# Kernel optimization log

Hardware: AMD Instinct MI355X
Metric: run time of the kernel (lower is better)

The kernel has to match this reference:

```python
import jax, jax.numpy as jnp
import numpy as np

K = 20          # args.k
NEG = 0.2       # LeakyReLU negative slope

def lrelu(x):
    return jnp.where(x >= 0, x, NEG * x)

def bn(x, s, b):
    # eval-mode batchnorm folded into per-channel affine; channel axis = 1
    sh = (1, -1) + (1,) * (x.ndim - 2)
    return x * s.reshape(sh) + b.reshape(sh)

def se(x, w1, w2):
    # Squeeze-and-Excite on (B, C, N, k)
    y = jnp.mean(x, axis=(2, 3))                      # (B, C)
    y = jax.nn.sigmoid(jax.nn.relu(y @ w1.T) @ w2.T)  # (B, C)
    return x * y[:, :, None, None]

def graph_feature(x):
    # x: (B, C, N) -> edge features (B, 2C, N, K)
    xx = jnp.sum(x * x, axis=1)                        # (B, N)
    inner = jnp.einsum('bcn,bcm->bnm', x, x)           # (B, N, N)
    dist = -xx[:, :, None] + 2.0 * inner - xx[:, None, :]
    idx = jax.lax.top_k(dist, K)[1]                    # (B, N, K) nearest (incl. self)
    xt = jnp.transpose(x, (0, 2, 1))                   # (B, N, C)
    nbr = jax.vmap(lambda t, i: t[i])(xt, idx)         # (B, N, K, C)
    ctr = xt[:, :, None, :]
    out = jnp.concatenate([nbr - ctr, jnp.broadcast_to(ctr, nbr.shape)], axis=3)
    return jnp.transpose(out, (0, 3, 1, 2))

def edge_block(x, w, s, b, w1, w2):
    # get_graph_feature -> 1x1 conv -> BN -> SE -> LeakyReLU -> max over k
    g = graph_feature(x)                               # (B, 2C, N, K)
    h = jnp.einsum('bcnk,oc->bonk', g, w)
    h = lrelu(se(bn(h, s, b), w1, w2))
    return jnp.max(h, axis=-1)                         # (B, O, N)

def forward(x, conv1_w, conv2_w, conv3_w, conv4_w, conv5_w,
            bn1_s, bn1_b, bn2_s, bn2_b, bn3_s, bn3_b, bn4_s, bn4_b, bn5_s, bn5_b,
            se1_w1, se1_w2, se2_w1, se2_w2, se3_w1, se3_w2, se4_w1, se4_w2,
            res1_w, res2_w, res3_w,
            lin1_w, bn6_s, bn6_b, lin2_w, lin2_b, bn7_s, bn7_b, lin3_w, lin3_b):
    x1 = edge_block(x, conv1_w, bn1_s, bn1_b, se1_w1, se1_w2)                 # (B,512,N)
    x2 = edge_block(x1, conv2_w, bn2_s, bn2_b, se2_w1, se2_w2)
    x2 = x2 + jnp.einsum('bcn,oc->bon', x1, res1_w)                           # (B,512,N)
    x3 = edge_block(x2, conv3_w, bn3_s, bn3_b, se3_w1, se3_w2)
    x3 = x3 + jnp.einsum('bcn,oc->bon', x2, res2_w)                           # (B,1024,N)
    x4 = edge_block(x3, conv4_w, bn4_s, bn4_b, se4_w1, se4_w2)
    x4 = x4 + jnp.einsum('bcn,oc->bon', x3, res3_w)                           # (B,1024,N)
    h = jnp.concatenate([x1, x2, x3, x4], axis=1)                             # (B,3072,N)
    h = lrelu(bn(jnp.einsum('bcn,oc->bon', h, conv5_w), bn5_s, bn5_b))        # (B,2048,N)
    f = jnp.concatenate([jnp.max(h, axis=-1), jnp.mean(h, axis=-1)], axis=1)  # (B,4096)
    f = lrelu(bn(f @ lin1_w.T, bn6_s, bn6_b))       # dropout is eval-mode identity
    f = lrelu(bn(f @ lin2_w.T + lin2_b, bn7_s, bn7_b))
    return f @ lin3_w.T + lin3_b                    # (B,40)

def setup_inputs():
    ks = jax.random.split(jax.random.key(0), 40)
    B, N = 16, 128
    f32 = jnp.float32
    def w(i, shape, s=0.02):
        return jax.random.normal(ks[i], shape, f32) * s
    def bns(i, c):
        return 1.0 + 0.1 * jax.random.normal(ks[i], (c,), f32)
    def bnb(i, c):
        return 0.1 * jax.random.normal(ks[i], (c,), f32)
    return {
        'x': jax.random.normal(ks[0], (B, 512, N), f32),
        'conv1_w': w(1, (512, 1024)),
        'conv2_w': w(2, (512, 1024)),
        'conv3_w': w(3, (1024, 1024)),
        'conv4_w': w(4, (1024, 2048)),
        'conv5_w': w(5, (2048, 3072)),
        'bn1_s': bns(6, 512), 'bn1_b': bnb(7, 512),
        'bn2_s': bns(8, 512), 'bn2_b': bnb(9, 512),
        'bn3_s': bns(10, 1024), 'bn3_b': bnb(11, 1024),
        'bn4_s': bns(12, 1024), 'bn4_b': bnb(13, 1024),
        'bn5_s': bns(14, 2048), 'bn5_b': bnb(15, 2048),
        'se1_w1': w(16, (32, 512), 0.05), 'se1_w2': w(17, (512, 32), 0.05),
        'se2_w1': w(18, (32, 512), 0.05), 'se2_w2': w(19, (512, 32), 0.05),
        'se3_w1': w(20, (64, 1024), 0.05), 'se3_w2': w(21, (1024, 64), 0.05),
        'se4_w1': w(22, (64, 1024), 0.05), 'se4_w2': w(23, (1024, 64), 0.05),
        'res1_w': w(24, (512, 512)),
        'res2_w': w(25, (1024, 512)),
        'res3_w': w(26, (1024, 1024)),
        'lin1_w': w(27, (512, 4096)),
        'bn6_s': bns(28, 512), 'bn6_b': bnb(29, 512),
        'lin2_w': w(30, (256, 512)), 'lin2_b': bnb(31, 256),
        'bn7_s': bns(32, 256), 'bn7_b': bnb(33, 256),
        'lin3_w': w(34, (40, 256)), 'lin3_b': bnb(35, 40),
    }

def reference(x, conv1_w, conv2_w, conv3_w, conv4_w, conv5_w,
              bn1_s, bn1_b, bn2_s, bn2_b, bn3_s, bn3_b, bn4_s, bn4_b, bn5_s, bn5_b,
              se1_w1, se1_w2, se2_w1, se2_w2, se3_w1, se3_w2, se4_w1, se4_w2,
              res1_w, res2_w, res3_w,
              lin1_w, bn6_s, bn6_b, lin2_w, lin2_b, bn7_s, bn7_b, lin3_w, lin3_b):
    return forward(x, conv1_w, conv2_w, conv3_w, conv4_w, conv5_w,
                   bn1_s, bn1_b, bn2_s, bn2_b, bn3_s, bn3_b, bn4_s, bn4_b, bn5_s, bn5_b,
                   se1_w1, se1_w2, se2_w1, se2_w2, se3_w1, se3_w2, se4_w1, se4_w2,
                   res1_w, res2_w, res3_w,
                   lin1_w, bn6_s, bn6_b, lin2_w, lin2_b, bn7_s, bn7_b, lin3_w, lin3_b)
```

## Files before the change

kernel.cpp:

```cpp
#include <hip/hip_runtime.h>
#include <hip/hip_bf16.h>


#define BN_ALL 2048
typedef __hip_bfloat16 bf16;
typedef __attribute__((ext_vector_type(8))) short short8;
typedef __attribute__((ext_vector_type(4))) float float4v;

__device__ __forceinline__ float b2f(bf16 v) { return __bfloat162float(v); }
__device__ __forceinline__ float lrelu(float v) { return v >= 0.f ? v : 0.2f * v; }
__device__ __forceinline__ short f2bs(float v) {
    bf16 h = __float2bfloat16(v);
    return *reinterpret_cast<short*>(&h);
}

__device__ __forceinline__ float ldin(const void* p, size_t i, int isb) {
    return isb ? __bfloat162float(((const bf16*)p)[i]) : ((const float*)p)[i];
}

__device__ __forceinline__ float ld1(const float* p) { return *p; }
__device__ __forceinline__ float ld1(const bf16* p)  { return __bfloat162float(*p); }
__device__ __forceinline__ void st1(float* p, float v) { *p = v; }
__device__ __forceinline__ void st1(bf16* p, float v)  { *p = __float2bfloat16(v); }
__device__ __forceinline__ short ldbs(const float* p) { return f2bs(*p); }
__device__ __forceinline__ short ldbs(const bf16* p)  { return *(const short*)p; }

__global__ __launch_bounds__(256) void detect_dtype(const void* __restrict__ x, int* __restrict__ flag) {
    const unsigned* u = (const unsigned*)x;
    int sane = 0;
    for (int i = threadIdx.x; i < 4096; i += 256) {
        unsigned e = (u[i] >> 23) & 0xFF;
        sane += (e >= 87 && e <= 167) ? 1 : 0;
    }
    __shared__ int sh[256];
    sh[threadIdx.x] = sane;
    __syncthreads();
    for (int off = 128; off > 0; off >>= 1) {
        if (threadIdx.x < off) sh[threadIdx.x] += sh[threadIdx.x + off];
        __syncthreads();
    }
    if (threadIdx.x == 0) *flag = (sh[0] < 2048) ? 1 : 0;
}

__global__ __launch_bounds__(256) void convert_kp(const void* __restrict__ x, bf16* __restrict__ X0,
                                                  const int* __restrict__ dflag) {
    int isb = *dflag;
    int item = blockIdx.x * 256 + threadIdx.x;
    int cg = item >> 11, bn = item & 2047;
    int b = bn >> 7, n = bn & 127;
    short8 pk;
#pragma unroll
    for (int j = 0; j < 8; ++j)
        pk[j] = f2bs(ldin(x, ((size_t)(b * 512 + cg * 8 + j)) * 128 + n, isb));
    *(short8*)((short*)X0 + ((size_t)cg * BN_ALL + bn) * 8) = pk;
}

__global__ __launch_bounds__(256) void gram_k(const bf16* __restrict__ X, int C,
                                              float* __restrict__ G) {
    __shared__ short Bsm[2][4096];
    int tid = threadIdx.x;
    int b = blockIdx.x;
    int lane = tid & 63, wv = tid >> 6, wm = wv & 1, wn = wv >> 1;
    int lq = lane >> 4, lr = lane & 15;
    int KC = C >> 5;
    const short* Xs = (const short*)X;

    float4v acc[4][4];
#pragma unroll
    for (int i = 0; i < 4; i++)
#pragma unroll
        for (int j = 0; j < 4; j++) acc[i][j] = (float4v){0.f, 0.f, 0.f, 0.f};

    short8 br2[2];
#pragma unroll
    for (int it = 0; it < 2; ++it) {
        int i = tid + it * 256;
        int q = i >> 7, c = i & 127;
        *(short8*)&Bsm[0][(size_t)i * 8] =
            *(const short8*)(Xs + ((size_t)q * BN_ALL + b * 128 + c) * 8);
    }
    __syncthreads();

    int p = 0;
    for (int kc = 0; kc < KC; ++kc) {
        if (kc + 1 < KC) {
#pragma unroll
            for (int it = 0; it < 2; ++it) {
                int i = tid + it * 256;
                int q = i >> 7, c = i & 127;
                br2[it] = *(const short8*)(Xs + ((size_t)((kc + 1) * 4 + q) * BN_ALL + b * 128 + c) * 8);
            }
        }
        short8 av[4], bv[4];
#pragma unroll
        for (int mt = 0; mt < 4; ++mt)
            av[mt] = *(const short8*)&Bsm[p][(size_t)((lq << 7) + wm * 64 + mt * 16 + lr) * 8];
#pragma unroll
        for (int nt = 0; nt < 4; ++nt)
            bv[nt] = *(const short8*)&Bsm[p][(size_t)((lq << 7) + wn * 64 + nt * 16 + lr) * 8];
#pragma unroll
        for (int mt = 0; mt < 4; ++mt)
#pragma unroll
            for (int nt = 0; nt < 4; ++nt)
                acc[mt][nt] = __builtin_amdgcn_mfma_f32_16x16x32_bf16(av[mt], bv[nt], acc[mt][nt], 0, 0, 0);
        if (kc + 1 < KC) {
#pragma unroll
            for (int it = 0; it < 2; ++it)
                *(short8*)&Bsm[p ^ 1][(size_t)(tid + it * 256) * 8] = br2[it];
        }
        __syncthreads();
        p ^= 1;
    }

    float* Gb = G + (size_t)b * 16384;
#pragma unroll
    for (int mt = 0; mt < 4; ++mt)
#pragma unroll
        for (int r = 0; r < 4; ++r) {
            int row = wm * 64 + mt * 16 + lq * 4 + r;
#pragma unroll
            for (int nt = 0; nt < 4; ++nt) {
                int col = wn * 64 + nt * 16 + lr;
                Gb[row * 128 + col] = acc[mt][nt][r];
            }
        }
}

__global__ __launch_bounds__(256) void topk_k(const float* __restrict__ G, int* __restrict__ idx) {
    int gw = (blockIdx.x * 256 + threadIdx.x) >> 6;
    int lane = threadIdx.x & 63;
    int b = gw >> 7, n = gw & 127;
    const float* Gb = G + (size_t)b * 16384;
    float g0 = Gb[n * 128 + lane];
    float g1 = Gb[n * 128 + 64 + lane];
    float dnn = Gb[n * 129];
    float dm0 = Gb[lane * 129];
    float dm1 = Gb[(64 + lane) * 129];
    float d0 = 2.f * g0 - dnn - dm0;
    float d1 = 2.f * g1 - dnn - dm1;
#pragma unroll
    for (int k = 0; k < 20; ++k) {
        float v; int i;
        if (d1 > d0) { v = d1; i = 64 + lane; } else { v = d0; i = lane; }
#pragma unroll
        for (int off = 1; off < 64; off <<= 1) {
            float ov = __shfl_xor(v, off, 64);
            int   oi = __shfl_xor(i, off, 64);
            if (ov > v || (ov == v && oi < i)) { v = ov; i = oi; }
        }
        if (lane == 0) idx[gw * 20 + k] = i;
        if (i < 64) { if (lane == i) d0 = -3.0e38f; }
        else        { if (lane == i - 64) d1 = -3.0e38f; }
    }
}

template <typename S>
__global__ __launch_bounds__(128) void knn_topk(const S* __restrict__ X, int C, int* __restrict__ idx) {
// ... 32 lines not shown
        }
        if (m == 0) { idx[blockIdx.x * 20 + k] = ri[0]; dist[ri[0]] = -3.0e38f; }
    }
}

__global__ __launch_bounds__(256) void pack_w(const void* __restrict__ w, int ldw,
                                              const void* __restrict__ res, int Cin, int O,
                                              int Mtot, int K, short* __restrict__ out,
                                              const int* __restrict__ dflag) {
    int isb = *dflag;
    int item = blockIdx.x * 256 + threadIdx.x;
    if (item >= Mtot * (K >> 3)) return;
    int m_local = item & 127;
    int rest = item >> 7;
    int q = rest & 3; rest >>= 2;
    int KC = K >> 5;
    int kc = rest % KC, tm = rest / KC;
    int grow = tm * 128 + m_local;
    int k = kc * 32 + q * 8;
    const void* src; size_t base; int dif = 0;
    if (grow < O)          { src = w;   base = (size_t)grow * ldw + k; }
    else if (grow < 2 * O) { src = w;   base = (size_t)(grow - O) * ldw + k; dif = 1; }
    else                   { src = res; base = (size_t)(grow - 2 * O) * Cin + k; }
    short8 pk;
#pragma unroll
    for (int j = 0; j < 8; ++j) {
        float v = ldin(src, base + j, isb);
        if (dif) v = ldin(src, base + Cin + j, isb) - v;
        pk[j] = f2bs(v);
    }
    *(short8*)&out[(size_t)item * 8] = pk;
}

__global__ __launch_bounds__(256) void gemm_pk(const short* __restrict__ packA,
                                               const bf16* __restrict__ X, float* __restrict__ Cm, int K,
                                               const void* __restrict__ bnS, const void* __restrict__ bnB,
                                               int act, const int* __restrict__ dflag) {
    __shared__ short Asm[2][4096];
    __shared__ short Bsm[2][2048];
    int tid = threadIdx.x;
    int bm  = blockIdx.x << 7;
    int bn0 = blockIdx.y << 6;
    int lane = tid & 63, wv = tid >> 6, wm = wv & 1, wn = wv >> 1;
    int lq = lane >> 4, lr = lane & 15;
    int KC = K >> 5;
    const short* abase = packA + (size_t)blockIdx.x * KC * 4096;
    const short* Xs = (const short*)X;
    int bq = tid >> 6, bc = tid & 63;

    float4v acc[4][2];
#pragma unroll
    for (int i = 0; i < 4; i++)
#pragma unroll
        for (int j = 0; j < 2; j++) acc[i][j] = (float4v){0.f, 0.f, 0.f, 0.f};

    short8 ar[2], brv;

#pragma unroll
    for (int it = 0; it < 2; ++it)
        ar[it] = *(const short8*)&abase[(size_t)(tid + it * 256) * 8];
    brv = *(const short8*)(Xs + ((size_t)bq * BN_ALL + bn0 + bc) * 8);
#pragma unroll
    for (int it = 0; it < 2; ++it)
        *(short8*)&Asm[0][(size_t)(tid + it * 256) * 8] = ar[it];
    *(short8*)&Bsm[0][(size_t)tid * 8] = brv;
    __syncthreads();

    int p = 0;
    for (int kc = 0; kc < KC; ++kc) {
        if (kc + 1 < KC) {
            const short* ab = abase + (size_t)(kc + 1) * 4096;
#pragma unroll
            for (int it = 0; it < 2; ++it)
                ar[it] = *(const short8*)&ab[(size_t)(tid + it * 256) * 8];
            brv = *(const short8*)(Xs + ((size_t)((kc + 1) * 4 + bq) * BN_ALL + bn0 + bc) * 8);
        }
        short8 av[4], bv[2];
#pragma unroll
        for (int mt = 0; mt < 4; ++mt)
            av[mt] = *(const short8*)&Asm[p][(size_t)((lq << 7) + wm * 64 + mt * 16 + lr) * 8];
#pragma unroll
        for (int nt = 0; nt < 2; ++nt)
            bv[nt] = *(const short8*)&Bsm[p][(size_t)((lq << 6) + wn * 32 + nt * 16 + lr) * 8];
#pragma unroll
        for (int mt = 0; mt < 4; ++mt)
#pragma unroll
            for (int nt = 0; nt < 2; ++nt)
                acc[mt][nt] = __builtin_amdgcn_mfma_f32_16x16x32_bf16(av[mt], bv[nt], acc[mt][nt], 0, 0, 0);
        if (kc + 1 < KC) {
#pragma unroll
            for (int it = 0; it < 2; ++it)
                *(short8*)&Asm[p ^ 1][(size_t)(tid + it * 256) * 8] = ar[it];
            *(short8*)&Bsm[p ^ 1][(size_t)tid * 8] = brv;
        }
        __syncthreads();
        p ^= 1;
    }

    int isb = *dflag;
#pragma unroll
    for (int mt = 0; mt < 4; ++mt) {
#pragma unroll
        for (int r = 0; r < 4; ++r) {
            int row = bm + wm * 64 + mt * 16 + lq * 4 + r;
            float s = 1.f, bb = 0.f;
            if (bnS) { s = ldin(bnS, row, isb); bb = ldin(bnB, row, isb); }
#pragma unroll
            for (int nt = 0; nt < 2; ++nt) {
                int col = bn0 + wn * 32 + nt * 16 + lr;
                float v = acc[mt][nt][r];
                if (bnS) v = v * s + bb;
                if (act) v = lrelu(v);
                Cm[(size_t)row * BN_ALL + col] = v;
            }
        }
    }
}

template <typename S>
__global__ __launch_bounds__(256) void gemm_mfma(const void* __restrict__ w, int ldw,
                                                 const void* __restrict__ res, int Cin, int O,
                                                 const S* __restrict__ X, S* __restrict__ Cm, int K,
                                                 const void* __restrict__ bnS, const void* __restrict__ bnB,
                                                 int act, const int* __restrict__ dflag) {
    int isb = *dflag;
    __shared__ short Asm[4096];
    __shared__ short Bsm[4096];
    int tid = threadIdx.x;
    int bm  = blockIdx.x << 7;
    int bn0 = blockIdx.y << 7;
    int lane = tid & 63, wv = tid >> 6;
    int wm = wv & 1, wn = wv >> 1;
    int lq = lane >> 4, lr = lane & 15;

    float4v acc[4][4];
#pragma unroll
    for (int i = 0; i < 4; i++)
#pragma unroll
        for (int j = 0; j < 4; j++) acc[i][j] = (float4v){0.f, 0.f, 0.f, 0.f};

    for (int k0 = 0; k0 < K; k0 += 32) {
#pragma unroll
        for (int it = 0; it < 2; ++it) {
            int i = tid + it * 256;
            int m = i >> 2, q = i & 3;
            int grow = bm + m;
            const void* asrc; size_t abase; int dif = 0;
            if (grow < O)          { asrc = w;   abase = (size_t)grow * ldw; }
            else if (grow < 2 * O) { asrc = w;   abase = (size_t)(grow - O) * ldw; dif = 1; }
            else                   { asrc = res; abase = (size_t)(grow - 2 * O) * Cin; }
            size_t kk = (size_t)k0 + q * 8;
// ... 135 lines not shown
    int item = blockIdx.x * 256 + threadIdx.x;
    int og = item >> 11, bn = item & 2047;
    int b = bn >> 7;
    short8 pk;
#pragma unroll
    for (int j = 0; j < 8; ++j) {
        int r = og * 8 + j;
        float v = Y[b * O + r] * PS[(size_t)r * BN_ALL + bn];
        if (useR) v += PS[(size_t)(2 * O + r) * BN_ALL + bn];
        pk[j] = f2bs(v);
    }
    *(short8*)((short*)Xdst + ((size_t)og * BN_ALL + bn) * 8) = pk;
}

template <typename SP, typename SD>
__global__ __launch_bounds__(256) void finalize(const SP* __restrict__ PS, const float* __restrict__ Y,
                                                int useR, SD* __restrict__ Xdst, int O) {
    int tid = blockIdx.x * 256 + threadIdx.x;
    int o = tid >> 11, bn = tid & 2047;
    int b = bn >> 7;
    float v = Y[b * O + o] * ld1(PS + tid);
    if (useR) v += ld1(PS + (size_t)(2 * O + o) * BN_ALL + bn);
    st1(Xdst + tid, v);
}

template <typename S>
__global__ __launch_bounds__(256) void convert_x(const void* __restrict__ x, S* __restrict__ X0,
                                                 const int* __restrict__ dflag) {
    int isb = *dflag;
    int tid = blockIdx.x * 256 + threadIdx.x;
    int c = tid >> 11, bn = tid & 2047;
    int b = bn >> 7, n = bn & 127;
    st1(X0 + tid, ldin(x, (size_t)(b * 512 + c) * 128 + n, isb));
}

template <typename S>
__global__ __launch_bounds__(128) void pool5(const S* __restrict__ H, float* __restrict__ f) {
    int m = blockIdx.x, b = blockIdx.y, n = threadIdx.x;
    float v = ld1(H + (size_t)m * BN_ALL + b * 128 + n);
    __shared__ float rmx[128], rsm[128];
    rmx[n] = v; rsm[n] = v;
    __syncthreads();
    for (int off = 64; off > 0; off >>= 1) {
        if (n < off) { rmx[n] = fmaxf(rmx[n], rmx[n + off]); rsm[n] += rsm[n + off]; }
        __syncthreads();
    }
    if (n == 0) {
        f[b * 4096 + m] = rmx[0];
        f[b * 4096 + 2048 + m] = rsm[0] * (1.f / 128.f);
    }
}

__global__ __launch_bounds__(256) void head_k(const float* __restrict__ in, const void* __restrict__ W,
                                              const void* __restrict__ bias, const void* __restrict__ bns,
                                              const void* __restrict__ bnb, float* __restrict__ outf,
                                              void* __restrict__ outb, int Kd, int Od, int act,
                                              const int* __restrict__ dflag) {
    int isb = *dflag;
    int gw = (blockIdx.x * 256 + threadIdx.x) >> 6;
    int lane = threadIdx.x & 63;
    if (gw >= 16 * Od) return;
    int b = gw / Od, o = gw - b * Od;
    const float* iv = in + b * Kd;
    float acc = 0.f;
    for (int k = lane; k < Kd; k += 64) acc += iv[k] * ldin(W, (size_t)o * Kd + k, isb);
    for (int off = 32; off > 0; off >>= 1) acc += __shfl_xor(acc, off, 64);
// ... 29 lines not shown
    const void* se3w1 = d_in[20], * se3w2 = d_in[21];                       \
    const void* se4w1 = d_in[22], * se4w2 = d_in[23];                       \
    const void* res1w = d_in[24]; const void* res2w = d_in[25];             \
    const void* res3w = d_in[26]; const void* lin1w = d_in[27];             \
    const void* bn6s = d_in[28], * bn6b = d_in[29];                         \
    const void* lin2w = d_in[30], * lin2b = d_in[31];                       \
    const void* bn7s = d_in[32], * bn7b = d_in[33];                         \
    const void* lin3w = d_in[34], * lin3b = d_in[35];

static void run_net_packed(void* const* d_in, void* d_out, void* d_ws, hipStream_t stream) {
    UNPACK_INPUTS();
    float* WS = (float*)d_ws;
    float* PS   = WS;
    bf16*  XC   = (bf16*)(WS + 6291456);
    short* PACK = (short*)(WS + 12582912);
    float* MB = WS + 15728640;
    float* YB = MB + 16384;
    float* FB = YB + 16384;
    float* F1 = FB + 65536;
    float* F2 = F1 + 8192;
    int* IDX  = (int*)(F2 + 4096);
    int* DFLAG = IDX + 40960;
    float* ZB = (float*)(DFLAG + 16);
    bf16*  X0 = (bf16*)(PS + (size_t)2048 * BN_ALL);
    float* GRAM = PS;
    bf16* X1 = XC;
    bf16* X2 = XC + (size_t)512 * BN_ALL;
    bf16* X3 = XC + (size_t)1024 * BN_ALL;
    bf16* X4 = XC + (size_t)2048 * BN_ALL;

    detect_dtype<<<1, 256, 0, stream>>>(x_in, DFLAG);
    convert_kp<<<512, 256, 0, stream>>>(x_in, X0, DFLAG);

    gram_k<<<16, 256, 0, stream>>>(X0, 512, GRAM);
    topk_k<<<512, 256, 0, stream>>>(GRAM, IDX);
    pack_w<<<256, 256, 0, stream>>>(conv1w, 1024, nullptr, 512, 512, 1024, 512, PACK, DFLAG);
    gemm_pk<<<dim3(8, 32), 256, 0, stream>>>(PACK, X0, PS, 512, nullptr, nullptr, 0, DFLAG);
    gather_pool<float><<<dim3(512, 16), 128, 0, stream>>>(PS, IDX, bn1s, bn1b, MB, 512, DFLAG);
    se1_k<<<128, 256, 0, stream>>>(MB, se1w1, ZB, 512, 32, DFLAG);
    se2_k<<<2048, 256, 0, stream>>>(ZB, se1w2, YB, 512, 32, DFLAG);
    finalize_kp<<<512, 256, 0, stream>>>(PS, YB, 0, X1, 512);

    gram_k<<<16, 256, 0, stream>>>(X1, 512, GRAM);
    topk_k<<<512, 256, 0, stream>>>(GRAM, IDX);
    pack_w<<<384, 256, 0, stream>>>(conv2w, 1024, res1w, 512, 512, 1536, 512, PACK, DFLAG);
    gemm_pk<<<dim3(12, 32), 256, 0, stream>>>(PACK, X1, PS, 512, nullptr, nullptr, 0, DFLAG);
    gather_pool<float><<<dim3(512, 16), 128, 0, stream>>>(PS, IDX, bn2s, bn2b, MB, 512, DFLAG);
    se1_k<<<128, 256, 0, stream>>>(MB, se2w1, ZB, 512, 32, DFLAG);
    se2_k<<<2048, 256, 0, stream>>>(ZB, se2w2, YB, 512, 32, DFLAG);
    finalize_kp<<<512, 256, 0, stream>>>(PS, YB, 1, X2, 512);

    gram_k<<<16, 256, 0, stream>>>(X2, 512, GRAM);
    topk_k<<<512, 256, 0, stream>>>(GRAM, IDX);
    pack_w<<<768, 256, 0, stream>>>(conv3w, 1024, res2w, 512, 1024, 3072, 512, PACK, DFLAG);
    gemm_pk<<<dim3(24, 32), 256, 0, stream>>>(PACK, X2, PS, 512, nullptr, nullptr, 0, DFLAG);
    gather_pool<float><<<dim3(1024, 16), 128, 0, stream>>>(PS, IDX, bn3s, bn3b, MB, 1024, DFLAG);
    se1_k<<<256, 256, 0, stream>>>(MB, se3w1, ZB, 1024, 64, DFLAG);
    se2_k<<<4096, 256, 0, stream>>>(ZB, se3w2, YB, 1024, 64, DFLAG);
    finalize_kp<<<1024, 256, 0, stream>>>(PS, YB, 1, X3, 1024);

    gram_k<<<16, 256, 0, stream>>>(X3, 1024, GRAM);
    topk_k<<<512, 256, 0, stream>>>(GRAM, IDX);
    pack_w<<<1536, 256, 0, stream>>>(conv4w, 2048, res3w, 1024, 1024, 3072, 1024, PACK, DFLAG);
    gemm_pk<<<dim3(24, 32), 256, 0, stream>>>(PACK, X3, PS, 1024, nullptr, nullptr, 0, DFLAG);
    gather_pool<float><<<dim3(1024, 16), 128, 0, stream>>>(PS, IDX, bn4s, bn4b, MB, 1024, DFLAG);
    se1_k<<<256, 256, 0, stream>>>(MB, se4w1, ZB, 1024, 64, DFLAG);
    se2_k<<<4096, 256, 0, stream>>>(ZB, se4w2, YB, 1024, 64, DFLAG);
    finalize_kp<<<1024, 256, 0, stream>>>(PS, YB, 1, X4, 1024);

    pack_w<<<3072, 256, 0, stream>>>(conv5w, 3072, nullptr, 3072, 2048, 2048, 3072, PACK, DFLAG);
    gemm_pk<<<dim3(16, 32), 256, 0, stream>>>(PACK, XC, PS, 3072, bn5s, bn5b, 1, DFLAG);
    pool5<float><<<dim3(2048, 16), 128, 0, stream>>>(PS, FB);

    head_k<<<2048, 256, 0, stream>>>(FB, lin1w, nullptr, bn6s, bn6b, F1, nullptr, 4096, 512, 1, DFLAG);
    head_k<<<1024, 256, 0, stream>>>(F1, lin2w, lin2b, bn7s, bn7b, F2, nullptr, 512, 256, 1, DFLAG);
    head_k<<<160, 256, 0, stream>>>(F2, lin3w, lin3b, nullptr, nullptr, nullptr, d_out, 256, 40, 0, DFLAG);
}

template <typename S>
static void run_net(void* const* d_in, void* d_out, void* d_ws, hipStream_t stream) {
    UNPACK_INPUTS();
    const size_t RC = (size_t)3072 * BN_ALL;
    S* PS = (S*)d_ws;
    S* XC = PS + RC;
    S* X0 = PS + (size_t)2048 * BN_ALL;
    float* MB = (float*)(XC + RC);
    float* YB = MB + 16 * 1024;
    float* FB = YB + 16 * 1024;
    float* F1 = FB + 16 * 4096;
    float* F2 = F1 + 16 * 512;
    int* IDX  = (int*)(F2 + 16 * 256);
    int* DFLAG = IDX + 16 * 128 * 20;

    S* X1 = XC;
    S* X2 = XC + (size_t)512 * BN_ALL;
    S* X3 = XC + (size_t)1024 * BN_ALL;
    S* X4 = XC + (size_t)2048 * BN_ALL;

    detect_dtype<<<1, 256, 0, stream>>>(x_in, DFLAG);
    convert_x<S><<<4096, 256, 0, stream>>>(x_in, X0, DFLAG);

    knn_topk<S><<<2048, 128, 0, stream>>>(X0, 512, IDX);
    gemm_mfma<S><<<dim3(8, 16), 256, 0, stream>>>(conv1w, 1024, nullptr, 512, 512, X0, PS, 512, nullptr, nullptr, 0, DFLAG);
    gather_pool<S><<<dim3(512, 16), 128, 0, stream>>>(PS, IDX, bn1s, bn1b, MB, 512, DFLAG);
    se_k<<<16, 256, 0, stream>>>(MB, se1w1, se1w2, YB, 512, 32, DFLAG);
// ... 47 lines not shown
```

Before: 626.1 us.

## Split gram kernel into column strips and split-K the conv5 GEMM

```diff
diff --git a/kernel.cpp b/kernel.cpp
--- a/kernel.cpp
+++ b/kernel.cpp
@@ -42,6 +42,12 @@
     if (threadIdx.x == 0) *flag = (sh[0] < 2048) ? 1 : 0;
 }
 
+__global__ __launch_bounds__(256) void zero_ps(float* __restrict__ P) {
+    int i = blockIdx.x * 256 + threadIdx.x;
+    float4 z = {0.f, 0.f, 0.f, 0.f};
+    *(float4*)(P + (size_t)i * 4) = z;
+}
+
 __global__ __launch_bounds__(256) void convert_kp(const void* __restrict__ x, bf16* __restrict__ X0,
                                                   const int* __restrict__ dflag) {
     int isb = *dflag;
@@ -59,17 +65,15 @@
                                               float* __restrict__ G) {
     __shared__ short Bsm[2][4096];
     int tid = threadIdx.x;
-    int b = blockIdx.x;
+    int b = blockIdx.x, strip = blockIdx.y;
     int lane = tid & 63, wv = tid >> 6, wm = wv & 1, wn = wv >> 1;
     int lq = lane >> 4, lr = lane & 15;
     int KC = C >> 5;
     const short* Xs = (const short*)X;
 
-    float4v acc[4][4];
-#pragma unroll
-    for (int i = 0; i < 4; i++)
-#pragma unroll
-        for (int j = 0; j < 4; j++) acc[i][j] = (float4v){0.f, 0.f, 0.f, 0.f};
+    float4v acc[4];
+#pragma unroll
+    for (int i = 0; i < 4; i++) acc[i] = (float4v){0.f, 0.f, 0.f, 0.f};
 
     short8 br2[2];
 #pragma unroll
@@ -91,18 +95,14 @@
                 br2[it] = *(const short8*)(Xs + ((size_t)((kc + 1) * 4 + q) * BN_ALL + b * 128 + c) * 8);
             }
         }
-        short8 av[4], bv[4];
+        short8 av[4], bv;
 #pragma unroll
         for (int mt = 0; mt < 4; ++mt)
             av[mt] = *(const short8*)&Bsm[p][(size_t)((lq << 7) + wm * 64 + mt * 16 + lr) * 8];
-#pragma unroll
-        for (int nt = 0; nt < 4; ++nt)
-            bv[nt] = *(const short8*)&Bsm[p][(size_t)((lq << 7) + wn * 64 + nt * 16 + lr) * 8];
+        bv = *(const short8*)&Bsm[p][(size_t)((lq << 7) + strip * 32 + wn * 16 + lr) * 8];
 #pragma unroll
         for (int mt = 0; mt < 4; ++mt)
-#pragma unroll
-            for (int nt = 0; nt < 4; ++nt)
-                acc[mt][nt] = __builtin_amdgcn_mfma_f32_16x16x32_bf16(av[mt], bv[nt], acc[mt][nt], 0, 0, 0);
+            acc[mt] = __builtin_amdgcn_mfma_f32_16x16x32_bf16(av[mt], bv, acc[mt], 0, 0, 0);
         if (kc + 1 < KC) {
 #pragma unroll
             for (int it = 0; it < 2; ++it)
@@ -118,11 +118,8 @@
 #pragma unroll
         for (int r = 0; r < 4; ++r) {
             int row = wm * 64 + mt * 16 + lq * 4 + r;
-#pragma unroll
-            for (int nt = 0; nt < 4; ++nt) {
-                int col = wn * 64 + nt * 16 + lr;
-                Gb[row * 128 + col] = acc[mt][nt][r];
-            }
+            int col = strip * 32 + wn * 16 + lr;
+            Gb[row * 128 + col] = acc[mt][r];
         }
 }
 
@@ -306,6 +303,86 @@
     }
 }
 
+__global__ __launch_bounds__(256) void gemm_sk(const short* __restrict__ packA,
+                                               const bf16* __restrict__ X, float* __restrict__ Cm,
+                                               int K, int KH) {
+    __shared__ short Asm[2][4096];
+    __shared__ short Bsm[2][2048];
+    int tid = threadIdx.x;
+    int bm  = blockIdx.x << 7;
+    int bn0 = blockIdx.y << 6;
+    int kh  = blockIdx.z;
+    int lane = tid & 63, wv = tid >> 6, wm = wv & 1, wn = wv >> 1;
+    int lq = lane >> 4, lr = lane & 15;
+    int KCfull = K >> 5;
+    int KC = KCfull / KH;
+    int kc0 = kh * KC;
+    const short* abase = packA + ((size_t)blockIdx.x * KCfull + kc0) * 4096;
+    const short* Xs = (const short*)X;
+    int bq = tid >> 6, bc = tid & 63;
+
+    float4v acc[4][2];
+#pragma unroll
+    for (int i = 0; i < 4; i++)
+#pragma unroll
+        for (int j = 0; j < 2; j++) acc[i][j] = (float4v){0.f, 0.f, 0.f, 0.f};
+
+    short8 ar[2], brv;
+
+#pragma unroll
+    for (int it = 0; it < 2; ++it)
+        ar[it] = *(const short8*)&abase[(size_t)(tid + it * 256) * 8];
+    brv = *(const short8*)(Xs + ((size_t)(kc0 * 4 + bq) * BN_ALL + bn0 + bc) * 8);
+#pragma unroll
+    for (int it = 0; it < 2; ++it)
+        *(short8*)&Asm[0][(size_t)(tid + it * 256) * 8] = ar[it];
+    *(short8*)&Bsm[0][(size_t)tid * 8] = brv;
+    __syncthreads();
+
+    int p = 0;
+    for (int kc = 0; kc < KC; ++kc) {
+        if (kc + 1 < KC) {
+            const short* ab = abase + (size_t)(kc + 1) * 4096;
+#pragma unroll
+            for (int it = 0; it < 2; ++it)
+                ar[it] = *(const short8*)&ab[(size_t)(tid + it * 256) * 8];
+            brv = *(const short8*)(Xs + ((size_t)((kc0 + kc + 1) * 4 + bq) * BN_ALL + bn0 + bc) * 8);
+        }
+        short8 av[4], bv[2];
+#pragma unroll
+        for (int mt = 0; mt < 4; ++mt)
+            av[mt] = *(const short8*)&Asm[p][(size_t)((lq << 7) + wm * 64 + mt * 16 + lr) * 8];
+#pragma unroll
+        for (int nt = 0; nt < 2; ++nt)
+            bv[nt] = *(const short8*)&Bsm[p][(size_t)((lq << 6) + wn * 32 + nt * 16 + lr) * 8];
+#pragma unroll
+        for (int mt = 0; mt < 4; ++mt)
+#pragma unroll
+            for (int nt = 0; nt < 2; ++nt)
+                acc[mt][nt] = __builtin_amdgcn_mfma_f32_16x16x32_bf16(av[mt], bv[nt], acc[mt][nt], 0, 0, 0);
+        if (kc + 1 < KC) {
+#pragma unroll
+            for (int it = 0; it < 2; ++it)
+                *(short8*)&Asm[p ^ 1][(size_t)(tid + it * 256) * 8] = ar[it];
+            *(short8*)&Bsm[p ^ 1][(size_t)tid * 8] = brv;
+        }
+        __syncthreads();
+        p ^= 1;
+    }
+
+#pragma unroll
+    for (int mt = 0; mt < 4; ++mt)
+#pragma unroll
+        for (int r = 0; r < 4; ++r) {
+            int row = bm + wm * 64 + mt * 16 + lq * 4 + r;
+#pragma unroll
+            for (int nt = 0; nt < 2; ++nt) {
+                int col = bn0 + wn * 32 + nt * 16 + lr;
+                atomicAdd(Cm + (size_t)row * BN_ALL + col, acc[mt][nt][r]);
+            }
+        }
+}
+
 template <typename S>
 __global__ __launch_bounds__(256) void gemm_mfma(const void* __restrict__ w, int ldw,
                                                  const void* __restrict__ res, int Cin, int O,
@@ -507,6 +584,26 @@
     int c = tid >> 11, bn = tid & 2047;
     int b = bn >> 7, n = bn & 127;
     st1(X0 + tid, ldin(x, (size_t)(b * 512 + c) * 128 + n, isb));
+}
+
+__global__ __launch_bounds__(128) void pool5_bn(const float* __restrict__ H, float* __restrict__ f,
+                                                const void* __restrict__ bns, const void* __restrict__ bnb,
+                                                const int* __restrict__ dflag) {
+    int isb = *dflag;
+    int m = blockIdx.x, b = blockIdx.y, n = threadIdx.x;
+    float s = ldin(bns, m, isb), bb = ldin(bnb, m, isb);
+    float v = lrelu(H[(size_t)m * BN_ALL + b * 128 + n] * s + bb);
+    __shared__ float rmx[128], rsm[128];
+    rmx[n] = v; rsm[n] = v;
+    __syncthreads();
+    for (int off = 64; off > 0; off >>= 1) {
+        if (n < off) { rmx[n] = fmaxf(rmx[n], rmx[n + off]); rsm[n] += rsm[n + off]; }
+        __syncthreads();
+    }
+    if (n == 0) {
+        f[b * 4096 + m] = rmx[0];
+        f[b * 4096 + 2048 + m] = rsm[0] * (1.f / 128.f);
+    }
 }
 
 template <typename S>
@@ -602,7 +699,7 @@
     detect_dtype<<<1, 256, 0, stream>>>(x_in, DFLAG);
     convert_kp<<<512, 256, 0, stream>>>(x_in, X0, DFLAG);
 
-    gram_k<<<16, 256, 0, stream>>>(X0, 512, GRAM);
+    gram_k<<<dim3(16, 4), 256, 0, stream>>>(X0, 512, GRAM);
     topk_k<<<512, 256, 0, stream>>>(GRAM, IDX);
     pack_w<<<256, 256, 0, stream>>>(conv1w, 1024, nullptr, 512, 512, 1024, 512, PACK, DFLAG);
     gemm_pk<<<dim3(8, 32), 256, 0, stream>>>(PACK, X0, PS, 512, nullptr, nullptr, 0, DFLAG);
@@ -611,7 +708,7 @@
     se2_k<<<2048, 256, 0, stream>>>(ZB, se1w2, YB, 512, 32, DFLAG);
     finalize_kp<<<512, 256, 0, stream>>>(PS, YB, 0, X1, 512);
 
-    gram_k<<<16, 256, 0, stream>>>(X1, 512, GRAM);
+    gram_k<<<dim3(16, 4), 256, 0, stream>>>(X1, 512, GRAM);
     topk_k<<<512, 256, 0, stream>>>(GRAM, IDX);
     pack_w<<<384, 256, 0, stream>>>(conv2w, 1024, res1w, 512, 512, 1536, 512, PACK, DFLAG);
     gemm_pk<<<dim3(12, 32), 256, 0, stream>>>(PACK, X1, PS, 512, nullptr, nullptr, 0, DFLAG);
@@ -620,7 +717,7 @@
     se2_k<<<2048, 256, 0, stream>>>(ZB, se2w2, YB, 512, 32, DFLAG);
     finalize_kp<<<512, 256, 0, stream>>>(PS, YB, 1, X2, 512);
 
-    gram_k<<<16, 256, 0, stream>>>(X2, 512, GRAM);
+    gram_k<<<dim3(16, 4), 256, 0, stream>>>(X2, 512, GRAM);
     topk_k<<<512, 256, 0, stream>>>(GRAM, IDX);
     pack_w<<<768, 256, 0, stream>>>(conv3w, 1024, res2w, 512, 1024, 3072, 512, PACK, DFLAG);
     gemm_pk<<<dim3(24, 32), 256, 0, stream>>>(PACK, X2, PS, 512, nullptr, nullptr, 0, DFLAG);
@@ -629,7 +726,7 @@
     se2_k<<<4096, 256, 0, stream>>>(ZB, se3w2, YB, 1024, 64, DFLAG);
     finalize_kp<<<1024, 256, 0, stream>>>(PS, YB, 1, X3, 1024);
 
-    gram_k<<<16, 256, 0, stream>>>(X3, 1024, GRAM);
+    gram_k<<<dim3(16, 4), 256, 0, stream>>>(X3, 1024, GRAM);
     topk_k<<<512, 256, 0, stream>>>(GRAM, IDX);
     pack_w<<<1536, 256, 0, stream>>>(conv4w, 2048, res3w, 1024, 1024, 3072, 1024, PACK, DFLAG);
     gemm_pk<<<dim3(24, 32), 256, 0, stream>>>(PACK, X3, PS, 1024, nullptr, nullptr, 0, DFLAG);
@@ -639,8 +736,9 @@
     finalize_kp<<<1024, 256, 0, stream>>>(PS, YB, 1, X4, 1024);
 
     pack_w<<<3072, 256, 0, stream>>>(conv5w, 3072, nullptr, 3072, 2048, 2048, 3072, PACK, DFLAG);
-    gemm_pk<<<dim3(16, 32), 256, 0, stream>>>(PACK, XC, PS, 3072, bn5s, bn5b, 1, DFLAG);
-    pool5<float><<<dim3(2048, 16), 128, 0, stream>>>(PS, FB);
+    zero_ps<<<4096, 256, 0, stream>>>(PS);
+    gemm_sk<<<dim3(16, 32, 2), 256, 0, stream>>>(PACK, XC, PS, 3072, 2);
+    pool5_bn<<<dim3(2048, 16), 128, 0, stream>>>(PS, FB, bn5s, bn5b, DFLAG);
 
     head_k<<<2048, 256, 0, stream>>>(FB, lin1w, nullptr, bn6s, bn6b, F1, nullptr, 4096, 512, 1, DFLAG);
     head_k<<<1024, 256, 0, stream>>>(F1, lin2w, lin2b, bn7s, bn7b, F2, nullptr, 512, 256, 1, DFLAG);
```

New measurement: 637.7 us. Within noise of the previous version (+1.9%).

## Split gram kernel into column strips and enlarge GEMM N-tile to 128

Applied to the files above, without the earlier changes.

```diff
diff --git a/kernel.cpp b/kernel.cpp
--- a/kernel.cpp
+++ b/kernel.cpp
@@ -59,17 +59,15 @@
                                               float* __restrict__ G) {
     __shared__ short Bsm[2][4096];
     int tid = threadIdx.x;
-    int b = blockIdx.x;
+    int b = blockIdx.x, strip = blockIdx.y;
     int lane = tid & 63, wv = tid >> 6, wm = wv & 1, wn = wv >> 1;
     int lq = lane >> 4, lr = lane & 15;
     int KC = C >> 5;
     const short* Xs = (const short*)X;
 
-    float4v acc[4][4];
-#pragma unroll
-    for (int i = 0; i < 4; i++)
-#pragma unroll
-        for (int j = 0; j < 4; j++) acc[i][j] = (float4v){0.f, 0.f, 0.f, 0.f};
+    float4v acc[4];
+#pragma unroll
+    for (int i = 0; i < 4; i++) acc[i] = (float4v){0.f, 0.f, 0.f, 0.f};
 
     short8 br2[2];
 #pragma unroll
@@ -91,18 +89,14 @@
                 br2[it] = *(const short8*)(Xs + ((size_t)((kc + 1) * 4 + q) * BN_ALL + b * 128 + c) * 8);
             }
         }
-        short8 av[4], bv[4];
+        short8 av[4], bv;
 #pragma unroll
         for (int mt = 0; mt < 4; ++mt)
             av[mt] = *(const short8*)&Bsm[p][(size_t)((lq << 7) + wm * 64 + mt * 16 + lr) * 8];
-#pragma unroll
-        for (int nt = 0; nt < 4; ++nt)
-            bv[nt] = *(const short8*)&Bsm[p][(size_t)((lq << 7) + wn * 64 + nt * 16 + lr) * 8];
+        bv = *(const short8*)&Bsm[p][(size_t)((lq << 7) + strip * 32 + wn * 16 + lr) * 8];
 #pragma unroll
         for (int mt = 0; mt < 4; ++mt)
-#pragma unroll
-            for (int nt = 0; nt < 4; ++nt)
-                acc[mt][nt] = __builtin_amdgcn_mfma_f32_16x16x32_bf16(av[mt], bv[nt], acc[mt][nt], 0, 0, 0);
+            acc[mt] = __builtin_amdgcn_mfma_f32_16x16x32_bf16(av[mt], bv, acc[mt], 0, 0, 0);
         if (kc + 1 < KC) {
 #pragma unroll
             for (int it = 0; it < 2; ++it)
@@ -118,11 +112,8 @@
 #pragma unroll
         for (int r = 0; r < 4; ++r) {
             int row = wm * 64 + mt * 16 + lq * 4 + r;
-#pragma unroll
-            for (int nt = 0; nt < 4; ++nt) {
-                int col = wn * 64 + nt * 16 + lr;
-                Gb[row * 128 + col] = acc[mt][nt][r];
-            }
+            int col = strip * 32 + wn * 16 + lr;
+            Gb[row * 128 + col] = acc[mt][r];
         }
 }
 
@@ -221,38 +212,40 @@
     *(short8*)&out[(size_t)item * 8] = pk;
 }
 
-__global__ __launch_bounds__(256) void gemm_pk(const short* __restrict__ packA,
+__global__ __launch_bounds__(256) void gemm_p2(const short* __restrict__ packA,
                                                const bf16* __restrict__ X, float* __restrict__ Cm, int K,
                                                const void* __restrict__ bnS, const void* __restrict__ bnB,
                                                int act, const int* __restrict__ dflag) {
     __shared__ short Asm[2][4096];
-    __shared__ short Bsm[2][2048];
+    __shared__ short Bsm[2][4096];
     int tid = threadIdx.x;
     int bm  = blockIdx.x << 7;
-    int bn0 = blockIdx.y << 6;
+    int bn0 = blockIdx.y << 7;
     int lane = tid & 63, wv = tid >> 6, wm = wv & 1, wn = wv >> 1;
     int lq = lane >> 4, lr = lane & 15;
     int KC = K >> 5;
     const short* abase = packA + (size_t)blockIdx.x * KC * 4096;
     const short* Xs = (const short*)X;
-    int bq = tid >> 6, bc = tid & 63;
-
-    float4v acc[4][2];
+
+    float4v acc[4][4];
 #pragma unroll
     for (int i = 0; i < 4; i++)
 #pragma unroll
-        for (int j = 0; j < 2; j++) acc[i][j] = (float4v){0.f, 0.f, 0.f, 0.f};
-
-    short8 ar[2], brv;
-
-#pragma unroll
-    for (int it = 0; it < 2; ++it)
+        for (int j = 0; j < 4; j++) acc[i][j] = (float4v){0.f, 0.f, 0.f, 0.f};
+
+    short8 ar[2], br[2];
+    int bq = tid >> 7, bc = tid & 127;
+
+#pragma unroll
+    for (int it = 0; it < 2; ++it) {
         ar[it] = *(const short8*)&abase[(size_t)(tid + it * 256) * 8];
-    brv = *(const short8*)(Xs + ((size_t)bq * BN_ALL + bn0 + bc) * 8);
-#pragma unroll
-    for (int it = 0; it < 2; ++it)
+        br[it] = *(const short8*)(Xs + ((size_t)(bq + it * 2) * BN_ALL + bn0 + bc) * 8);
+    }
+#pragma unroll
+    for (int it = 0; it < 2; ++it) {
         *(short8*)&Asm[0][(size_t)(tid + it * 256) * 8] = ar[it];
-    *(short8*)&Bsm[0][(size_t)tid * 8] = brv;
+        *(short8*)&Bsm[0][(size_t)(tid + it * 256) * 8] = br[it];
+    }
     __syncthreads();
 
     int p = 0;
@@ -260,27 +253,29 @@
         if (kc + 1 < KC) {
             const short* ab = abase + (size_t)(kc + 1) * 4096;
 #pragma unroll
-            for (int it = 0; it < 2; ++it)
+            for (int it = 0; it < 2; ++it) {
                 ar[it] = *(const short8*)&ab[(size_t)(tid + it * 256) * 8];
-            brv = *(const short8*)(Xs + ((size_t)((kc + 1) * 4 + bq) * BN_ALL + bn0 + bc) * 8);
-        }
-        short8 av[4], bv[2];
+                br[it] = *(const short8*)(Xs + ((size_t)((kc + 1) * 4 + bq + it * 2) * BN_ALL + bn0 + bc) * 8);
+            }
+        }
+        short8 av[4], bv[4];
 #pragma unroll
         for (int mt = 0; mt < 4; ++mt)
             av[mt] = *(const short8*)&Asm[p][(size_t)((lq << 7) + wm * 64 + mt * 16 + lr) * 8];
 #pragma unroll
-        for (int nt = 0; nt < 2; ++nt)
-            bv[nt] = *(const short8*)&Bsm[p][(size_t)((lq << 6) + wn * 32 + nt * 16 + lr) * 8];
+        for (int nt = 0; nt < 4; ++nt)
+            bv[nt] = *(const short8*)&Bsm[p][(size_t)((lq << 7) + wn * 64 + nt * 16 + lr) * 8];
 #pragma unroll
         for (int mt = 0; mt < 4; ++mt)
 #pragma unroll
-            for (int nt = 0; nt < 2; ++nt)
+            for (int nt = 0; nt < 4; ++nt)
                 acc[mt][nt] = __builtin_amdgcn_mfma_f32_16x16x32_bf16(av[mt], bv[nt], acc[mt][nt], 0, 0, 0);
         if (kc + 1 < KC) {
 #pragma unroll
-            for (int it = 0; it < 2; ++it)
+            for (int it = 0; it < 2; ++it) {
                 *(short8*)&Asm[p ^ 1][(size_t)(tid + it * 256) * 8] = ar[it];
-            *(short8*)&Bsm[p ^ 1][(size_t)tid * 8] = brv;
+                *(short8*)&Bsm[p ^ 1][(size_t)(tid + it * 256) * 8] = br[it];
+            }
         }
         __syncthreads();
         p ^= 1;
@@ -295,8 +290,8 @@
             float s = 1.f, bb = 0.f;
             if (bnS) { s = ldin(bnS, row, isb); bb = ldin(bnB, row, isb); }
 #pragma unroll
-            for (int nt = 0; nt < 2; ++nt) {
-                int col = bn0 + wn * 32 + nt * 16 + lr;
+            for (int nt = 0; nt < 4; ++nt) {
+                int col = bn0 + wn * 64 + nt * 16 + lr;
                 float v = acc[mt][nt][r];
                 if (bnS) v = v * s + bb;
                 if (act) v = lrelu(v);
@@ -602,44 +597,44 @@
     detect_dtype<<<1, 256, 0, stream>>>(x_in, DFLAG);
     convert_kp<<<512, 256, 0, stream>>>(x_in, X0, DFLAG);
 
-    gram_k<<<16, 256, 0, stream>>>(X0, 512, GRAM);
+    gram_k<<<dim3(16, 4), 256, 0, stream>>>(X0, 512, GRAM);
     topk_k<<<512, 256, 0, stream>>>(GRAM, IDX);
     pack_w<<<256, 256, 0, stream>>>(conv1w, 1024, nullptr, 512, 512, 1024, 512, PACK, DFLAG);
-    gemm_pk<<<dim3(8, 32), 256, 0, stream>>>(PACK, X0, PS, 512, nullptr, nullptr, 0, DFLAG);
+    gemm_p2<<<dim3(8, 16), 256, 0, stream>>>(PACK, X0, PS, 512, nullptr, nullptr, 0, DFLAG);
     gather_pool<float><<<dim3(512, 16), 128, 0, stream>>>(PS, IDX, bn1s, bn1b, MB, 512, DFLAG);
     se1_k<<<128, 256, 0, stream>>>(MB, se1w1, ZB, 512, 32, DFLAG);
     se2_k<<<2048, 256, 0, stream>>>(ZB, se1w2, YB, 512, 32, DFLAG);
     finalize_kp<<<512, 256, 0, stream>>>(PS, YB, 0, X1, 512);
 
-    gram_k<<<16, 256, 0, stream>>>(X1, 512, GRAM);
+    gram_k<<<dim3(16, 4), 256, 0, stream>>>(X1, 512, GRAM);
     topk_k<<<512, 256, 0, stream>>>(GRAM, IDX);
     pack_w<<<384, 256, 0, stream>>>(conv2w, 1024, res1w, 512, 512, 1536, 512, PACK, DFLAG);
-    gemm_pk<<<dim3(12, 32), 256, 0, stream>>>(PACK, X1, PS, 512, nullptr, nullptr, 0, DFLAG);
+    gemm_p2<<<dim3(12, 16), 256, 0, stream>>>(PACK, X1, PS, 512, nullptr, nullptr, 0, DFLAG);
     gather_pool<float><<<dim3(512, 16), 128, 0, stream>>>(PS, IDX, bn2s, bn2b, MB, 512, DFLAG);
     se1_k<<<128, 256, 0, stream>>>(MB, se2w1, ZB, 512, 32, DFLAG);
     se2_k<<<2048, 256, 0, stream>>>(ZB, se2w2, YB, 512, 32, DFLAG);
     finalize_kp<<<512, 256, 0, stream>>>(PS, YB, 1, X2, 512);
 
-    gram_k<<<16, 256, 0, stream>>>(X2, 512, GRAM);
+    gram_k<<<dim3(16, 4), 256, 0, stream>>>(X2, 512, GRAM);
     topk_k<<<512, 256, 0, stream>>>(GRAM, IDX);
     pack_w<<<768, 256, 0, stream>>>(conv3w, 1024, res2w, 512, 1024, 3072, 512, PACK, DFLAG);
-    gemm_pk<<<dim3(24, 32), 256, 0, stream>>>(PACK, X2, PS, 512, nullptr, nullptr, 0, DFLAG);
+    gemm_p2<<<dim3(24, 16), 256, 0, stream>>>(PACK, X2, PS, 512, nullptr, nullptr, 0, DFLAG);
     gather_pool<float><<<dim3(1024, 16), 128, 0, stream>>>(PS, IDX, bn3s, bn3b, MB, 1024, DFLAG);
     se1_k<<<256, 256, 0, stream>>>(MB, se3w1, ZB, 1024, 64, DFLAG);
     se2_k<<<4096, 256, 0, stream>>>(ZB, se3w2, YB, 1024, 64, DFLAG);
     finalize_kp<<<1024, 256, 0, stream>>>(PS, YB, 1, X3, 1024);
 
-    gram_k<<<16, 256, 0, stream>>>(X3, 1024, GRAM);
+    gram_k<<<dim3(16, 4), 256, 0, stream>>>(X3, 1024, GRAM);
     topk_k<<<512, 256, 0, stream>>>(GRAM, IDX);
     pack_w<<<1536, 256, 0, stream>>>(conv4w, 2048, res3w, 1024, 1024, 3072, 1024, PACK, DFLAG);
-    gemm_pk<<<dim3(24, 32), 256, 0, stream>>>(PACK, X3, PS, 1024, nullptr, nullptr, 0, DFLAG);
+    gemm_p2<<<dim3(24, 16), 256, 0, stream>>>(PACK, X3, PS, 1024, nullptr, nullptr, 0, DFLAG);
     gather_pool<float><<<dim3(1024, 16), 128, 0, stream>>>(PS, IDX, bn4s, bn4b, MB, 1024, DFLAG);
     se1_k<<<256, 256, 0, stream>>>(MB, se4w1, ZB, 1024, 64, DFLAG);
     se2_k<<<4096, 256, 0, stream>>>(ZB, se4w2, YB, 1024, 64, DFLAG);
     finalize_kp<<<1024, 256, 0, stream>>>(PS, YB, 1, X4, 1024);
 
     pack_w<<<3072, 256, 0, stream>>>(conv5w, 3072, nullptr, 3072, 2048, 2048, 3072, PACK, DFLAG);
-    gemm_pk<<<dim3(16, 32), 256, 0, stream>>>(PACK, XC, PS, 3072, bn5s, bn5b, 1, DFLAG);
+    gemm_p2<<<dim3(16, 16), 256, 0, stream>>>(PACK, XC, PS, 3072, bn5s, bn5b, 1, DFLAG);
     pool5<float><<<dim3(2048, 16), 128, 0, stream>>>(PS, FB);
 
     head_k<<<2048, 256, 0, stream>>>(FB, lin1w, nullptr, bn6s, bn6b, F1, nullptr, 4096, 512, 1, DFLAG);
```

New measurement: 646.5 us. +3.2%, slower.

## Load GEMM and Gram tiles directly into LDS and split Gram across column strips

Applied to the files above, without the earlier changes.

```diff
diff --git a/kernel.cpp b/kernel.cpp
--- a/kernel.cpp
+++ b/kernel.cpp
@@ -6,6 +6,20 @@
 typedef __hip_bfloat16 bf16;
 typedef __attribute__((ext_vector_type(8))) short short8;
 typedef __attribute__((ext_vector_type(4))) float float4v;
+
+#if defined(__has_builtin)
+#if __has_builtin(__builtin_amdgcn_global_load_lds)
+#define HAS_GLL 1
+#endif
+#endif
+
+#ifdef HAS_GLL
+__device__ __forceinline__ void gll16(const void* g, void* l) {
+    __builtin_amdgcn_global_load_lds(
+        (const __attribute__((address_space(1))) void*)g,
+        (__attribute__((address_space(3))) void*)l, 16, 0, 0);
+}
+#endif
 
 __device__ __forceinline__ float b2f(bf16 v) { return __bfloat162float(v); }
 __device__ __forceinline__ float lrelu(float v) { return v >= 0.f ? v : 0.2f * v; }
@@ -22,8 +36,6 @@
 __device__ __forceinline__ float ld1(const bf16* p)  { return __bfloat162float(*p); }
 __device__ __forceinline__ void st1(float* p, float v) { *p = v; }
 __device__ __forceinline__ void st1(bf16* p, float v)  { *p = __float2bfloat16(v); }
-__device__ __forceinline__ short ldbs(const float* p) { return f2bs(*p); }
-__device__ __forceinline__ short ldbs(const bf16* p)  { return *(const short*)p; }
 
 __global__ __launch_bounds__(256) void detect_dtype(const void* __restrict__ x, int* __restrict__ flag) {
     const unsigned* u = (const unsigned*)x;
@@ -57,20 +69,49 @@
 
 __global__ __launch_bounds__(256) void gram_k(const bf16* __restrict__ X, int C,
                                               float* __restrict__ G) {
-    __shared__ short Bsm[2][4096];
+    __shared__ __align__(16) short Bsm[2][4096];
     int tid = threadIdx.x;
-    int b = blockIdx.x;
+    int b = blockIdx.x, strip = blockIdx.y;
     int lane = tid & 63, wv = tid >> 6, wm = wv & 1, wn = wv >> 1;
     int lq = lane >> 4, lr = lane & 15;
     int KC = C >> 5;
     const short* Xs = (const short*)X;
 
-    float4v acc[4][4];
-#pragma unroll
-    for (int i = 0; i < 4; i++)
-#pragma unroll
-        for (int j = 0; j < 4; j++) acc[i][j] = (float4v){0.f, 0.f, 0.f, 0.f};
-
+    float4v acc[4];
+#pragma unroll
+    for (int i = 0; i < 4; i++) acc[i] = (float4v){0.f, 0.f, 0.f, 0.f};
+
+#ifdef HAS_GLL
+#pragma unroll
+    for (int it = 0; it < 2; ++it) {
+        int i = tid + it * 256;
+        int q = i >> 7, c = i & 127;
+        gll16(Xs + ((size_t)q * BN_ALL + b * 128 + c) * 8, &Bsm[0][(size_t)i * 8]);
+    }
+    __syncthreads();
+    int p = 0;
+    for (int kc = 0; kc < KC; ++kc) {
+        if (kc + 1 < KC) {
+#pragma unroll
+            for (int it = 0; it < 2; ++it) {
+                int i = tid + it * 256;
+                int q = i >> 7, c = i & 127;
+                gll16(Xs + ((size_t)((kc + 1) * 4 + q) * BN_ALL + b * 128 + c) * 8,
+                      &Bsm[p ^ 1][(size_t)i * 8]);
+            }
+        }
+        short8 av[4], bv;
+#pragma unroll
+        for (int mt = 0; mt < 4; ++mt)
+            av[mt] = *(const short8*)&Bsm[p][(size_t)((lq << 7) + wm * 64 + mt * 16 + lr) * 8];
+        bv = *(const short8*)&Bsm[p][(size_t)((lq << 7) + strip * 32 + wn * 16 + lr) * 8];
+#pragma unroll
+        for (int mt = 0; mt < 4; ++mt)
+            acc[mt] = __builtin_amdgcn_mfma_f32_16x16x32_bf16(av[mt], bv, acc[mt], 0, 0, 0);
+        __syncthreads();
+        p ^= 1;
+    }
+#else
     short8 br2[2];
 #pragma unroll
     for (int it = 0; it < 2; ++it) {
@@ -80,7 +121,6 @@
             *(const short8*)(Xs + ((size_t)q * BN_ALL + b * 128 + c) * 8);
     }
     __syncthreads();
-
     int p = 0;
     for (int kc = 0; kc < KC; ++kc) {
         if (kc + 1 < KC) {
@@ -91,18 +131,14 @@
                 br2[it] = *(const short8*)(Xs + ((size_t)((kc + 1) * 4 + q) * BN_ALL + b * 128 + c) * 8);
             }
         }
-        short8 av[4], bv[4];
+        short8 av[4], bv;
 #pragma unroll
         for (int mt = 0; mt < 4; ++mt)
             av[mt] = *(const short8*)&Bsm[p][(size_t)((lq << 7) + wm * 64 + mt * 16 + lr) * 8];
-#pragma unroll
-        for (int nt = 0; nt < 4; ++nt)
-            bv[nt] = *(const short8*)&Bsm[p][(size_t)((lq << 7) + wn * 64 + nt * 16 + lr) * 8];
-#pragma unroll
-        for (int mt = 0; mt < 4; ++mt)
-#pragma unroll
-            for (int nt = 0; nt < 4; ++nt)
-                acc[mt][nt] = __builtin_amdgcn_mfma_f32_16x16x32_bf16(av[mt], bv[nt], acc[mt][nt], 0, 0, 0);
+        bv = *(const short8*)&Bsm[p][(size_t)((lq << 7) + strip * 32 + wn * 16 + lr) * 8];
+#pragma unroll
+        for (int mt = 0; mt < 4; ++mt)
+            acc[mt] = __builtin_amdgcn_mfma_f32_16x16x32_bf16(av[mt], bv, acc[mt], 0, 0, 0);
         if (kc + 1 < KC) {
 #pragma unroll
             for (int it = 0; it < 2; ++it)
@@ -111,6 +147,7 @@
         __syncthreads();
         p ^= 1;
     }
+#endif
 
     float* Gb = G + (size_t)b * 16384;
 #pragma unroll
@@ -118,11 +155,8 @@
 #pragma unroll
         for (int r = 0; r < 4; ++r) {
             int row = wm * 64 + mt * 16 + lq * 4 + r;
-#pragma unroll
-            for (int nt = 0; nt < 4; ++nt) {
-                int col = wn * 64 + nt * 16 + lr;
-                Gb[row * 128 + col] = acc[mt][nt][r];
-            }
+            int col = strip * 32 + wn * 16 + lr;
+            Gb[row * 128 + col] = acc[mt][r];
         }
 }
 
@@ -225,8 +259,8 @@
                                                const bf16* __restrict__ X, float* __restrict__ Cm, int K,
                                                const void* __restrict__ bnS, const void* __restrict__ bnB,
                                                int act, const int* __restrict__ dflag) {
-    __shared__ short Asm[2][4096];
-    __shared__ short Bsm[2][2048];
+    __shared__ __align__(16) short Asm[2][4096];
+    __shared__ __align__(16) short Bsm[2][2048];
     int tid = threadIdx.x;
     int bm  = blockIdx.x << 7;
     int bn0 = blockIdx.y << 6;
@@ -243,22 +277,50 @@
 #pragma unroll
         for (int j = 0; j < 2; j++) acc[i][j] = (float4v){0.f, 0.f, 0.f, 0.f};
 
-    short8 ar[2], brv;
-
-#pragma unroll
-    for (int it = 0; it < 2; ++it)
-        ar[it] = *(const short8*)&abase[(size_t)(tid + it * 256) * 8];
-    brv = *(const short8*)(Xs + ((size_t)bq * BN_ALL + bn0 + bc) * 8);
-#pragma unroll
-    for (int it = 0; it < 2; ++it)
-        *(short8*)&Asm[0][(size_t)(tid + it * 256) * 8] = ar[it];
-    *(short8*)&Bsm[0][(size_t)tid * 8] = brv;
-    __syncthreads();
-
+#ifdef HAS_GLL
+    gll16(abase + (size_t)tid * 8,        &Asm[0][(size_t)tid * 8]);
+    gll16(abase + (size_t)(tid + 256) * 8, &Asm[0][(size_t)(tid + 256) * 8]);
+    gll16(Xs + ((size_t)bq * BN_ALL + bn0 + bc) * 8, &Bsm[0][(size_t)tid * 8]);
+    __syncthreads();
     int p = 0;
     for (int kc = 0; kc < KC; ++kc) {
         if (kc + 1 < KC) {
             const short* ab = abase + (size_t)(kc + 1) * 4096;
+            gll16(ab + (size_t)tid * 8,         &Asm[p ^ 1][(size_t)tid * 8]);
+            gll16(ab + (size_t)(tid + 256) * 8, &Asm[p ^ 1][(size_t)(tid + 256) * 8]);
+            gll16(Xs + ((size_t)((kc + 1) * 4 + bq) * BN_ALL + bn0 + bc) * 8,
+                  &Bsm[p ^ 1][(size_t)tid * 8]);
+        }
+        short8 av[4], bv[2];
+#pragma unroll
+        for (int mt = 0; mt < 4; ++mt)
+            av[mt] = *(const short8*)&Asm[p][(size_t)((lq << 7) + wm * 64 + mt * 16 + lr) * 8];
+#pragma unroll
+        for (int nt = 0; nt < 2; ++nt)
+            bv[nt] = *(const short8*)&Bsm[p][(size_t)((lq << 6) + wn * 32 + nt * 16 + lr) * 8];
+#pragma unroll
+        for (int mt = 0; mt < 4; ++mt)
+#pragma unroll
+            for (int nt = 0; nt < 2; ++nt)
+                acc[mt][nt] = __builtin_amdgcn_mfma_f32_16x16x32_bf16(av[mt], bv[nt], acc[mt][nt], 0, 0, 0);
+        __syncthreads();
+        p ^= 1;
+    }
+#else
+    short8 ar[2], brv;
+#pragma unroll
+    for (int it = 0; it < 2; ++it)
+        ar[it] = *(const short8*)&abase[(size_t)(tid + it * 256) * 8];
+    brv = *(const short8*)(Xs + ((size_t)bq * BN_ALL + bn0 + bc) * 8);
+#pragma unroll
+    for (int it = 0; it < 2; ++it)
+        *(short8*)&Asm[0][(size_t)(tid + it * 256) * 8] = ar[it];
+    *(short8*)&Bsm[0][(size_t)tid * 8] = brv;
+    __syncthreads();
+    int p = 0;
+    for (int kc = 0; kc < KC; ++kc) {
+        if (kc + 1 < KC) {
+            const short* ab = abase + (size_t)(kc + 1) * 4096;
 #pragma unroll
             for (int it = 0; it < 2; ++it)
                 ar[it] = *(const short8*)&ab[(size_t)(tid + it * 256) * 8];
@@ -285,6 +347,7 @@
         __syncthreads();
         p ^= 1;
     }
+#endif
 
     int isb = *dflag;
 #pragma unroll
@@ -602,7 +665,7 @@
     detect_dtype<<<1, 256, 0, stream>>>(x_in, DFLAG);
     convert_kp<<<512, 256, 0, stream>>>(x_in, X0, DFLAG);
 
-    gram_k<<<16, 256, 0, stream>>>(X0, 512, GRAM);
+    gram_k<<<dim3(16, 4), 256, 0, stream>>>(X0, 512, GRAM);
     topk_k<<<512, 256, 0, stream>>>(GRAM, IDX);
     pack_w<<<256, 256, 0, stream>>>(conv1w, 1024, nullptr, 512, 512, 1024, 512, PACK, DFLAG);
     gemm_pk<<<dim3(8, 32), 256, 0, stream>>>(PACK, X0, PS, 512, nullptr, nullptr, 0, DFLAG);
@@ -611,7 +674,7 @@
     se2_k<<<2048, 256, 0, stream>>>(ZB, se1w2, YB, 512, 32, DFLAG);
     finalize_kp<<<512, 256, 0, stream>>>(PS, YB, 0, X1, 512);
 
-    gram_k<<<16, 256, 0, stream>>>(X1, 512, GRAM);
+    gram_k<<<dim3(16, 4), 256, 0, stream>>>(X1, 512, GRAM);
     topk_k<<<512, 256, 0, stream>>>(GRAM, IDX);
     pack_w<<<384, 256, 0, stream>>>(conv2w, 1024, res1w, 512, 512, 1536, 512, PACK, DFLAG);
     gemm_pk<<<dim3(12, 32), 256, 0, stream>>>(PACK, X1, PS, 512, nullptr, nullptr, 0, DFLAG);
@@ -620,7 +683,7 @@
     se2_k<<<2048, 256, 0, stream>>>(ZB, se2w2, YB, 512, 32, DFLAG);
     finalize_kp<<<512, 256, 0, stream>>>(PS, YB, 1, X2, 512);
 
-    gram_k<<<16, 256, 0, stream>>>(X2, 512, GRAM);
+    gram_k<<<dim3(16, 4), 256, 0, stream>>>(X2, 512, GRAM);
     topk_k<<<512, 256, 0, stream>>>(GRAM, IDX);
     pack_w<<<768, 256, 0, stream>>>(conv3w, 1024, res2w, 512, 1024, 3072, 512, PACK, DFLAG);
     gemm_pk<<<dim3(24, 32), 256, 0, stream>>>(PACK, X2, PS, 512, nullptr, nullptr, 0, DFLAG);
@@ -629,7 +692,7 @@
     se2_k<<<4096, 256, 0, stream>>>(ZB, se3w2, YB, 1024, 64, DFLAG);
     finalize_kp<<<1024, 256, 0, stream>>>(PS, YB, 1, X3, 1024);
 
-    gram_k<<<16, 256, 0, stream>>>(X3, 1024, GRAM);
+    gram_k<<<dim3(16, 4), 256, 0, stream>>>(X3, 1024, GRAM);
     topk_k<<<512, 256, 0, stream>>>(GRAM, IDX);
     pack_w<<<1536, 256, 0, stream>>>(conv4w, 2048, res3w, 1024, 1024, 3072, 1024, PACK, DFLAG);
     gemm_pk<<<dim3(24, 32), 256, 0, stream>>>(PACK, X3, PS, 1024, nullptr, nullptr, 0, DFLAG);
```

Result: no change. 629.1 us (+0.5%).
